# Kernel tuning notes

Measured on AMD Instinct MI355X. Metric: run time of the kernel, lower is better.

The kernel has to match this reference:

```python
import jax, jax.numpy as jnp
import numpy as np

D_MODEL = 768
N_HEADS = 12
D_K = D_MODEL // N_HEADS


def setup_inputs() -> dict:
    key = jax.random.key(0)
    ks = jax.random.split(key, 11)
    B, T = 4, 2048
    s = 1.0 / np.sqrt(D_K)
    so = 1.0 / np.sqrt(D_MODEL)
    return {
        "q": jax.random.normal(ks[0], (B, T, D_MODEL), jnp.float32),
        "k": jax.random.normal(ks[1], (B, T, D_MODEL), jnp.float32),
        "v": jax.random.normal(ks[2], (B, T, D_MODEL), jnp.float32),
        "Wq": jax.random.normal(ks[3], (D_K, D_K), jnp.float32) * s,
        "bq": jax.random.normal(ks[4], (D_K,), jnp.float32) * s,
        "Wk": jax.random.normal(ks[5], (D_K, D_K), jnp.float32) * s,
        "bk": jax.random.normal(ks[6], (D_K,), jnp.float32) * s,
        "Wv": jax.random.normal(ks[7], (D_K, D_K), jnp.float32) * s,
        "bv": jax.random.normal(ks[8], (D_K,), jnp.float32) * s,
        "Wo": jax.random.normal(ks[9], (D_MODEL, D_MODEL), jnp.float32) * so,
        "bo": jax.random.normal(ks[10], (D_MODEL,), jnp.float32) * so,
    }


def reference(q, k, v, Wq, bq, Wk, bk, Wv, bv, Wo, bo):
    B, T, _ = q.shape
    # split into heads: [B, T, H, d_k]; per-head Linear shares weights across heads
    qh = q.reshape(B, T, N_HEADS, D_K)
    kh = k.reshape(B, T, N_HEADS, D_K)
    vh = v.reshape(B, T, N_HEADS, D_K)
    # torch Linear: x @ W^T + b, then transpose to [B, H, T, d_k]
    qh = jnp.einsum("bthd,ed->bhte", qh, Wq) + bq
    kh = jnp.einsum("bthd,ed->bhte", kh, Wk) + bk
    vh = jnp.einsum("bthd,ed->bhte", vh, Wv) + bv
    # scaled dot-product attention, full [B,H,T,T] scores (faithful to source)
    scores = jnp.einsum("bhqd,bhkd->bhqk", qh, kh) / jnp.sqrt(
        jnp.asarray(D_K, qh.dtype)
    )
    attn = jax.nn.softmax(scores, axis=-1)
    # einsum 'ijkl,ijlr->ikjr' -> output laid out [B, T, H, d_k]
    out_h = jnp.einsum("bhqk,bhkd->bqhd", attn, vh)
    concat = out_h.reshape(B, T, D_MODEL)
    return concat @ Wo.T + bo
```

## Files before the change

### kernel.cpp

```cpp
#include <hip/hip_runtime.h>


#define T_SEQ  2048
#define NH     12
#define DK     64
#define DMODEL 768
#define BATCH  4

typedef __attribute__((ext_vector_type(8))) short short8;
typedef __attribute__((ext_vector_type(4))) float f32x4;
typedef __attribute__((ext_vector_type(4))) unsigned short us4;

#define CEXP (0.125f * 1.44269504088896340736f)

__device__ __forceinline__ unsigned cvt_pk_bf16(float lo, float hi) {
  unsigned r;
  asm("v_cvt_pk_bf16_f32 %0, %1, %2" : "=v"(r) : "v"(lo), "v"(hi));
  return r;
}
__device__ __forceinline__ unsigned short f2bf1(float f) {
  unsigned r;
  asm("v_cvt_pk_bf16_f32 %0, %1, %1" : "=v"(r) : "v"(f));
  return (unsigned short)r;
}
__device__ __forceinline__ us4 f4_to_bf4(float4 v) {
  union { unsigned u[2]; us4 r; } t;
  t.u[0] = cvt_pk_bf16(v.x, v.y);
  t.u[1] = cvt_pk_bf16(v.z, v.w);
  return t.r;
}


__global__ __launch_bounds__(256, 4)
void qkv_proj_kernel(const float* __restrict__ qin,
                     const float* __restrict__ kin,
                     const float* __restrict__ vin,
                     const float* __restrict__ Wq, const float* __restrict__ bq,
                     const float* __restrict__ Wk, const float* __restrict__ bk,
                     const float* __restrict__ Wv, const float* __restrict__ bv,
                     unsigned short* __restrict__ Qp,
                     unsigned short* __restrict__ Kp,
                     unsigned short* __restrict__ Vt)
{
  const int tt  = blockIdx.x;
  const int bh  = blockIdx.y;
  const int p   = blockIdx.z;
  const int b   = bh / NH, h = bh % NH;
  const int t0  = tt * 128;
  const int tid = threadIdx.x;
  const int wv  = tid >> 6;
  const int ln  = tid & 63;
  const int c   = ln & 15;
  const int qd  = ln >> 4;

  __shared__ __align__(16) unsigned short sX[128 * 72];
  __shared__ __align__(16) unsigned short sW[64 * 72];

  const float* in = (p == 0) ? qin : (p == 1) ? kin : vin;
  const float* W  = (p == 0) ? Wq  : (p == 1) ? Wk  : Wv;
  const float* bs = (p == 0) ? bq  : (p == 1) ? bk  : bv;

  const int r0 = tid >> 4, g = tid & 15;
#pragma unroll
  for (int l = 0; l < 8; ++l) {
    int r = l * 16 + r0;
    float4 xv = *reinterpret_cast<const float4*>(in + ((size_t)(b * T_SEQ + t0 + r)) * DMODEL + h * DK + g * 4);
    *reinterpret_cast<us4*>(&sX[r * 72 + g * 4]) = f4_to_bf4(xv);
  }
#pragma unroll
  for (int l = 0; l < 4; ++l) {
    int r = l * 16 + r0;
    float4 wvv = *reinterpret_cast<const float4*>(W + r * DK + g * 4);
    *reinterpret_cast<us4*>(&sW[r * 72 + g * 4]) = f4_to_bf4(wvv);
  }
  __syncthreads();

  short8 af[2][2];
#pragma unroll
  for (int f = 0; f < 2; ++f)
#pragma unroll
    for (int kc = 0; kc < 2; ++kc)
      af[f][kc] = *reinterpret_cast<const short8*>(&sX[(wv * 32 + f * 16 + c) * 72 + kc * 32 + qd * 8]);

  f32x4 acc[2][4];
#pragma unroll
  for (int nb = 0; nb < 4; ++nb) {
    short8 b0 = *reinterpret_cast<const short8*>(&sW[(nb * 16 + c) * 72 + qd * 8]);
    short8 b1 = *reinterpret_cast<const short8*>(&sW[(nb * 16 + c) * 72 + 32 + qd * 8]);
#pragma unroll
    for (int f = 0; f < 2; ++f) {
      f32x4 a = {0.f, 0.f, 0.f, 0.f};
      a = __builtin_amdgcn_mfma_f32_16x16x32_bf16(af[f][0], b0, a, 0, 0, 0);
      a = __builtin_amdgcn_mfma_f32_16x16x32_bf16(af[f][1], b1, a, 0, 0, 0);
      acc[f][nb] = a;
    }
  }

  __syncthreads();

  if (p < 2) {
    unsigned short* outp = (p == 0) ? Qp : Kp;
    const float sc = (p == 0) ? CEXP : 1.0f;
#pragma unroll
    for (int f = 0; f < 2; ++f)
#pragma unroll
      for (int nb = 0; nb < 4; ++nb) {
        int n = nb * 16 + c;
        float bias = bs[n] * sc;
#pragma unroll
        for (int r = 0; r < 4; ++r) {
          int row = wv * 32 + f * 16 + qd * 4 + r;
          sX[row * 68 + n] = f2bf1(fmaf(acc[f][nb][r], sc, bias));
        }
      }
    __syncthreads();
#pragma unroll
    for (int l = 0; l < 8; ++l) {
      int idx = l * 256 + tid;
      int r  = idx >> 4;
      int g2 = idx & 15;
      us4 val = *reinterpret_cast<const us4*>(&sX[r * 68 + g2 * 4]);
      *reinterpret_cast<us4*>(outp + ((size_t)bh * T_SEQ + t0 + r) * DK + g2 * 4) = val;
    }
  } else {
#pragma unroll
    for (int f = 0; f < 2; ++f)
#pragma unroll
      for (int nb = 0; nb < 4; ++nb) {
        int n = nb * 16 + c;
        float bias = bs[n];
#pragma unroll
        for (int r = 0; r < 4; ++r) {
          int row = wv * 32 + f * 16 + qd * 4 + r;
          sX[n * 136 + row] = f2bf1(acc[f][nb][r] + bias);
        }
      }
    __syncthreads();
#pragma unroll
    for (int l = 0; l < 8; ++l) {
      int idx = l * 256 + tid;
      int d  = idx >> 5;
      int gg = idx & 31;
      us4 val = *reinterpret_cast<const us4*>(&sX[d * 136 + gg * 4]);
      *reinterpret_cast<us4*>(Vt + ((size_t)bh * DK + d) * T_SEQ + t0 + gg * 4) = val;
    }
  }
}

__global__ __launch_bounds__(256, 3)
void flash_kernel(const unsigned short* __restrict__ Qp,
                  const unsigned short* __restrict__ Kp,
                  const unsigned short* __restrict__ Vt,
                  unsigned short* __restrict__ concat)
{
  const int lin = blockIdx.y * 16 + blockIdx.x;
  const int xcd = lin & 7;
  const int li  = lin >> 3;
  const int bh  = xcd * 6 + (li >> 4);
  const int qt  = li & 15;
  const int b   = bh / NH, h = bh % NH;
  const int tid = threadIdx.x;
  const int wv  = tid >> 6;
  const int ln  = tid & 63;
  const int c   = ln & 15;
  const int qd  = ln >> 4;

  __shared__ __align__(16) unsigned short sK[2][64 * 72];
  __shared__ __align__(16) unsigned short sV[2][64 * 72];

  const int row0 = qt * 128 + wv * 32;

  short8 qf[2][2];
#pragma unroll
  for (int f = 0; f < 2; ++f) {
    const unsigned short* qb = Qp + ((size_t)bh * T_SEQ + row0 + f * 16 + c) * DK + qd * 8;
    qf[f][0] = *reinterpret_cast<const short8*>(qb);
    qf[f][1] = *reinterpret_cast<const short8*>(qb + 32);
  }

  const int r0 = tid >> 4, g = tid & 15;
  us4 kreg[4], vreg[4];
#define LOAD_TILE(J)                                                                   \
  {                                                                                    \
    _Pragma("unroll")                                                                  \
    for (int l_ = 0; l_ < 4; ++l_) {                                                   \
      int r_ = l_ * 16 + r0;                                                           \
      kreg[l_] = *reinterpret_cast<const us4*>(Kp + ((size_t)bh * T_SEQ + (J) * 64 + r_) * DK + g * 4); \
      vreg[l_] = *reinterpret_cast<const us4*>(Vt + ((size_t)bh * DK + r_) * T_SEQ + (J) * 64 + g * 4); \
    }                                                                                  \
  }
#define WRITE_BUF(B)                                                                   \
  {                                                                                    \
    _Pragma("unroll")                                                                  \
    for (int l_ = 0; l_ < 4; ++l_) {                                                   \
      int r_ = l_ * 16 + r0;                                                           \
      *reinterpret_cast<us4*>(&sK[B][r_ * 72 + g * 4]) = kreg[l_];                     \
      *reinterpret_cast<us4*>(&sV[B][r_ * 72 + g * 4]) = vreg[l_];                     \
    }                                                                                  \
  }

  LOAD_TILE(0);
  WRITE_BUF(0);
  LOAD_TILE(1);

  f32x4 o[2][4];
  f32x4 lacc[2];
#pragma unroll
  for (int f = 0; f < 2; ++f) {
    lacc[f] = (f32x4){0.f, 0.f, 0.f, 0.f};
#pragma unroll
    for (int nb = 0; nb < 4; ++nb) o[f][nb] = (f32x4){0.f, 0.f, 0.f, 0.f};
  }

  short8 ones;
#pragma unroll
  for (int i = 0; i < 8; ++i) ones[i] = (short)0x3F80;

  for (int j = 0; j < T_SEQ / 64; ++j) {
    __syncthreads();
    const int cur = j & 1;
    WRITE_BUF((j + 1) & 1);
    LOAD_TILE((j + 2) & (T_SEQ / 64 - 1));

    short8 kf[4][2];
#pragma unroll
    for (int nb = 0; nb < 4; ++nb) {
      kf[nb][0] = *reinterpret_cast<const short8*>(&sK[cur][(nb * 16 + c) * 72 + qd * 8]);
      kf[nb][1] = *reinterpret_cast<const short8*>(&sK[cur][(nb * 16 + c) * 72 + 32 + qd * 8]);
    }

    short8 pf[2][2];
#pragma unroll
    for (int f = 0; f < 2; ++f) {
      f32x4 stf[4];
#pragma unroll
      for (int nb = 0; nb < 4; ++nb) {
        f32x4 a = {0.f, 0.f, 0.f, 0.f};
        a = __builtin_amdgcn_mfma_f32_16x16x32_bf16(kf[nb][0], qf[f][0], a, 0, 0, 0);
        a = __builtin_amdgcn_mfma_f32_16x16x32_bf16(kf[nb][1], qf[f][1], a, 0, 0, 0);
        stf[nb] = a;
      }
      unsigned pk[4][2];
#pragma unroll
      for (int nb = 0; nb < 4; ++nb) {
        float p0 = __builtin_amdgcn_exp2f(stf[nb][0]);
        float p1 = __builtin_amdgcn_exp2f(stf[nb][1]);
        float p2 = __builtin_amdgcn_exp2f(stf[nb][2]);
        float p3 = __builtin_amdgcn_exp2f(stf[nb][3]);
        pk[nb][0] = cvt_pk_bf16(p0, p1);
        pk[nb][1] = cvt_pk_bf16(p2, p3);
      }
#pragma unroll
      for (int kc = 0; kc < 2; ++kc) {
        union { unsigned w[4]; short8 s; } u;
#pragma unroll
        for (int pr = 0; pr < 2; ++pr) {
          unsigned X = pk[2 * kc][pr];
          unsigned Y = pk[2 * kc + 1][pr];
          auto s32 = __builtin_amdgcn_permlane32_swap(X, Y, false, false);
          auto s16 = __builtin_amdgcn_permlane16_swap(s32[0], s32[1], false, false);
          u.w[pr]     = s16[0];
          u.w[2 + pr] = s16[1];
        }
        pf[f][kc] = u.s;
      }
    }

    short8 vf[4][2];
#pragma unroll
    for (int nb = 0; nb < 4; ++nb) {
      vf[nb][0] = *reinterpret_cast<const short8*>(&sV[cur][(nb * 16 + c) * 72 + qd * 8]);
      vf[nb][1] = *reinterpret_cast<const short8*>(&sV[cur][(nb * 16 + c) * 72 + 32 + qd * 8]);
    }

#pragma unroll
    for (int f = 0; f < 2; ++f) {
      lacc[f] = __builtin_amdgcn_mfma_f32_16x16x32_bf16(pf[f][0], ones, lacc[f], 0, 0, 0);
      lacc[f] = __builtin_amdgcn_mfma_f32_16x16x32_bf16(pf[f][1], ones, lacc[f], 0, 0, 0);
    }

#pragma unroll
    for (int f = 0; f < 2; ++f)
#pragma unroll
      for (int nb = 0; nb < 4; ++nb) {
        o[f][nb] = __builtin_amdgcn_mfma_f32_16x16x32_bf16(pf[f][0], vf[nb][0], o[f][nb], 0, 0, 0);
        o[f][nb] = __builtin_amdgcn_mfma_f32_16x16x32_bf16(pf[f][1], vf[nb][1], o[f][nb], 0, 0, 0);
      }
  }

#pragma unroll
  for (int f = 0; f < 2; ++f) {
    float linv[4];
#pragma unroll
    for (int r = 0; r < 4; ++r) linv[r] = __builtin_amdgcn_rcpf(lacc[f][r]);
#pragma unroll
    for (int r = 0; r < 4; ++r) {
      int t = row0 + f * 16 + qd * 4 + r;
#pragma unroll
      for (int nb = 0; nb < 4; ++nb) {
        concat[((size_t)(b * T_SEQ + t)) * DMODEL + h * DK + nb * 16 + c] =
            f2bf1(o[f][nb][r] * linv[r]);
      }
    }
  }
#undef LOAD_TILE
#undef WRITE_BUF
}

__global__ __launch_bounds__(256, 3)
void oproj_kernel(const unsigned short* __restrict__ A,
                  const float* __restrict__ Wo,
                  const float* __restrict__ bo,
                  float* __restrict__ out)
{
  const int nt  = blockIdx.x;
  const int mt  = blockIdx.y;
  const int tid = threadIdx.x;
  const int wv  = tid >> 6;
  const int ln  = tid & 63;
  const int c   = ln & 15;
  const int qd  = ln >> 4;

  __shared__ __align__(16) unsigned short sA[128 * 72];
  __shared__ __align__(16) unsigned short sB[64 * 72];

  const int r0 = tid >> 4, g = tid & 15;
  us4 areg[8];
  float4 breg[4];
#define LOAD_K(KK)                                                                       \
  {                                                                                      \
    _Pragma("unroll")                                                                    \
    for (int l = 0; l < 8; ++l)                                                          \
      areg[l] = *reinterpret_cast<const us4*>(A + ((size_t)(mt * 128 + l * 16 + r0)) * DMODEL + (KK) * 64 + g * 4); \
    _Pragma("unroll")                                                                    \
    for (int l = 0; l < 4; ++l)                                                          \
      breg[l] = *reinterpret_cast<const float4*>(Wo + ((size_t)(nt * 64 + l * 16 + r0)) * DMODEL + (KK) * 64 + g * 4); \
  }

  LOAD_K(0);

  f32x4 acc[2][4];
#pragma unroll
  for (int f = 0; f < 2; ++f)
#pragma unroll
    for (int nb = 0; nb < 4; ++nb) acc[f][nb] = (f32x4){0.f, 0.f, 0.f, 0.f};

  for (int kk = 0; kk < DMODEL / 64; ++kk) {
    __syncthreads();
#pragma unroll
    for (int l = 0; l < 8; ++l)
      *reinterpret_cast<us4*>(&sA[(l * 16 + r0) * 72 + g * 4]) = areg[l];
#pragma unroll
    for (int l = 0; l < 4; ++l)
      *reinterpret_cast<us4*>(&sB[(l * 16 + r0) * 72 + g * 4]) = f4_to_bf4(breg[l]);
    __syncthreads();

    int kn = kk + 1 < DMODEL / 64 ? kk + 1 : 0;
    LOAD_K(kn);

    short8 af[2][2];
#pragma unroll
    for (int f = 0; f < 2; ++f) {
      af[f][0] = *reinterpret_cast<const short8*>(&sA[(wv * 32 + f * 16 + c) * 72 + qd * 8]);
      af[f][1] = *reinterpret_cast<const short8*>(&sA[(wv * 32 + f * 16 + c) * 72 + 32 + qd * 8]);
    }
#pragma unroll
    for (int nb = 0; nb < 4; ++nb) {
      short8 b0 = *reinterpret_cast<const short8*>(&sB[(nb * 16 + c) * 72 + qd * 8]);
      short8 b1 = *reinterpret_cast<const short8*>(&sB[(nb * 16 + c) * 72 + 32 + qd * 8]);
#pragma unroll
      for (int f = 0; f < 2; ++f) {
        acc[f][nb] = __builtin_amdgcn_mfma_f32_16x16x32_bf16(af[f][0], b0, acc[f][nb], 0, 0, 0);
        acc[f][nb] = __builtin_amdgcn_mfma_f32_16x16x32_bf16(af[f][1], b1, acc[f][nb], 0, 0, 0);
      }
    }
  }

#pragma unroll
  for (int f = 0; f < 2; ++f)
#pragma unroll
    for (int nb = 0; nb < 4; ++nb) {
      int n = nt * 64 + nb * 16 + c;
      float bias = bo[n];
#pragma unroll
      for (int r = 0; r < 4; ++r) {
        int m = mt * 128 + wv * 32 + f * 16 + qd * 4 + r;
        out[(size_t)m * DMODEL + n] = acc[f][nb][r] + bias;
      }
    }
#undef LOAD_K
}

extern "C" void kernel_launch(void* const* d_in, const int* in_sizes, int n_in,
                              void* d_out, int out_size, void* d_ws, size_t ws_size,
                              hipStream_t stream) {
  const float* q  = (const float*)d_in[0];
  const float* k  = (const float*)d_in[1];
  const float* v  = (const float*)d_in[2];
  const float* Wq = (const float*)d_in[3];
  const float* bq = (const float*)d_in[4];
  const float* Wk = (const float*)d_in[5];
  const float* bk = (const float*)d_in[6];
  const float* Wv = (const float*)d_in[7];
  const float* bv = (const float*)d_in[8];
  const float* Wo = (const float*)d_in[9];
  const float* bo = (const float*)d_in[10];

  const size_t NTOK = (size_t)BATCH * T_SEQ;
  const size_t PER  = NTOK * DK * NH;
  unsigned short* Qp     = (unsigned short*)d_ws;
  unsigned short* Kp     = Qp + PER;
  unsigned short* Vt     = Kp + PER;
  unsigned short* concat = Vt + PER;

  dim3 blk(256);
  qkv_proj_kernel<<<dim3(16, BATCH * NH, 3), blk, 0, stream>>>(q, k, v, Wq, bq, Wk, bk, Wv, bv, Qp, Kp, Vt);
  flash_kernel<<<dim3(16, BATCH * NH), blk, 0, stream>>>(Qp, Kp, Vt, concat);
  oproj_kernel<<<dim3(12, 64), blk, 0, stream>>>(concat, Wo, bo, (float*)d_out);
}
```

Measured before the change: 213.7 us.

## Stage K/V tiles via direct global-to-LDS loads with XOR-swizzled layout

The flash kernel's K and V tiles are now copied straight from global memory into LDS with global_load_lds 16-byte loads, replacing the register round-trip of load, hold and store. The padded 72-stride LDS layout becomes an unpadded 64-stride layout with an XOR swizzle on the column to avoid bank conflicts. This removes VGPRs and VALU/LDS store instructions used for staging and reduces the pipeline to one-tile-ahead prefetch. The risk is that the single __syncthreads may not wait for the asynchronous LDS writes (no explicit vmcnt wait), and the prefetch distance is shorter than before.

```diff
diff --git a/kernel.cpp b/kernel.cpp
--- a/kernel.cpp
+++ b/kernel.cpp
@@ -28,6 +28,12 @@
   t.u[0] = cvt_pk_bf16(v.x, v.y);
   t.u[1] = cvt_pk_bf16(v.z, v.w);
   return t.r;
+}
+
+__device__ __forceinline__ void gl_lds16(const void* g, void* l) {
+  __builtin_amdgcn_global_load_lds(
+      (const __attribute__((address_space(1))) void*)g,
+      (__attribute__((address_space(3))) void*)l, 16, 0, 0);
 }
 
 
@@ -165,8 +171,8 @@
   const int c   = ln & 15;
   const int qd  = ln >> 4;
 
-  __shared__ __align__(16) unsigned short sK[2][64 * 72];
-  __shared__ __align__(16) unsigned short sV[2][64 * 72];
+  __shared__ __align__(16) unsigned short sK[2][64 * 64];
+  __shared__ __align__(16) unsigned short sV[2][64 * 64];
 
   const int row0 = qt * 128 + wv * 32;
 
@@ -178,30 +184,28 @@
     qf[f][1] = *reinterpret_cast<const short8*>(qb + 32);
   }
 
-  const int r0 = tid >> 4, g = tid & 15;
-  us4 kreg[4], vreg[4];
-#define LOAD_TILE(J)                                                                   \
-  {                                                                                    \
-    _Pragma("unroll")                                                                  \
-    for (int l_ = 0; l_ < 4; ++l_) {                                                   \
-      int r_ = l_ * 16 + r0;                                                           \
-      kreg[l_] = *reinterpret_cast<const us4*>(Kp + ((size_t)bh * T_SEQ + (J) * 64 + r_) * DK + g * 4); \
-      vreg[l_] = *reinterpret_cast<const us4*>(Vt + ((size_t)bh * DK + r_) * T_SEQ + (J) * 64 + g * 4); \
-    }                                                                                  \
-  }
-#define WRITE_BUF(B)                                                                   \
-  {                                                                                    \
-    _Pragma("unroll")                                                                  \
-    for (int l_ = 0; l_ < 4; ++l_) {                                                   \
-      int r_ = l_ * 16 + r0;                                                           \
-      *reinterpret_cast<us4*>(&sK[B][r_ * 72 + g * 4]) = kreg[l_];                     \
-      *reinterpret_cast<us4*>(&sV[B][r_ * 72 + g * 4]) = vreg[l_];                     \
-    }                                                                                  \
-  }
-
-  LOAD_TILE(0);
-  WRITE_BUF(0);
-  LOAD_TILE(1);
+  int srow[2], scolb[2], schunk[2];
+#pragma unroll
+  for (int i = 0; i < 2; ++i) {
+    schunk[i] = wv * 2 + i;
+    int p = schunk[i] * 1024 + ln * 16;
+    int l = p ^ (((p >> 7) & 7) << 4);
+    srow[i]  = l >> 7;
+    scolb[i] = l & 127;
+  }
+
+#define STAGE(J, B)                                                                     \
+  {                                                                                     \
+    _Pragma("unroll")                                                                   \
+    for (int i_ = 0; i_ < 2; ++i_) {                                                    \
+      const char* ks_ = (const char*)(Kp + ((size_t)bh * T_SEQ + (J) * 64 + srow[i_]) * DK) + scolb[i_]; \
+      gl_lds16(ks_, &sK[B][schunk[i_] * 512]);                                          \
+      const char* vs_ = (const char*)(Vt + ((size_t)bh * DK + srow[i_]) * T_SEQ + (J) * 64) + scolb[i_]; \
+      gl_lds16(vs_, &sV[B][schunk[i_] * 512]);                                          \
+    }                                                                                   \
+  }
+
+  STAGE(0, 0);
 
   f32x4 o[2][4];
   f32x4 lacc[2];
@@ -215,18 +219,19 @@
   short8 ones;
 #pragma unroll
   for (int i = 0; i < 8; ++i) ones[i] = (short)0x3F80;
+
+  const int sw = (c & 7) << 3;
 
   for (int j = 0; j < T_SEQ / 64; ++j) {
     __syncthreads();
     const int cur = j & 1;
-    WRITE_BUF((j + 1) & 1);
-    LOAD_TILE((j + 2) & (T_SEQ / 64 - 1));
+    STAGE((j + 1) & (T_SEQ / 64 - 1), cur ^ 1);
 
     short8 kf[4][2];
 #pragma unroll
     for (int nb = 0; nb < 4; ++nb) {
-      kf[nb][0] = *reinterpret_cast<const short8*>(&sK[cur][(nb * 16 + c) * 72 + qd * 8]);
-      kf[nb][1] = *reinterpret_cast<const short8*>(&sK[cur][(nb * 16 + c) * 72 + 32 + qd * 8]);
+      kf[nb][0] = *reinterpret_cast<const short8*>(&sK[cur][(nb * 16 + c) * 64 + ((0 * 32 + qd * 8) ^ sw)]);
+      kf[nb][1] = *reinterpret_cast<const short8*>(&sK[cur][(nb * 16 + c) * 64 + ((1 * 32 + qd * 8) ^ sw)]);
     }
 
     short8 pf[2][2];
@@ -269,8 +274,8 @@
     short8 vf[4][2];
 #pragma unroll
     for (int nb = 0; nb < 4; ++nb) {
-      vf[nb][0] = *reinterpret_cast<const short8*>(&sV[cur][(nb * 16 + c) * 72 + qd * 8]);
-      vf[nb][1] = *reinterpret_cast<const short8*>(&sV[cur][(nb * 16 + c) * 72 + 32 + qd * 8]);
+      vf[nb][0] = *reinterpret_cast<const short8*>(&sV[cur][(nb * 16 + c) * 64 + ((0 * 32 + qd * 8) ^ sw)]);
+      vf[nb][1] = *reinterpret_cast<const short8*>(&sV[cur][(nb * 16 + c) * 64 + ((1 * 32 + qd * 8) ^ sw)]);
     }
 
 #pragma unroll
@@ -303,8 +308,7 @@
       }
     }
   }
-#undef LOAD_TILE
-#undef WRITE_BUF
+#undef STAGE
 }
 
 __global__ __launch_bounds__(256, 3)
```

After: 217.0 us. No clear change (+1.5%).
